# Performance work log

Hardware: AMD Instinct MI355X
Metric: run time of the kernel (lower is better)

The kernel has to match this reference:

```python
import jax, jax.numpy as jnp
import numpy as np

EPS = 1e-5
KS = 3
PAD = 1


def _bn(x, g, b, m, v):
    inv = g / jnp.sqrt(v + EPS)
    return x * inv[None, :, None, None] + (b - m * inv)[None, :, None, None]


def _deform_conv2d(x, off_w, off_b, w):
    # x: (B,C,H,W); off_w: (2*9,C,3,3); w: (Cout,C,3,3)
    B, C, H, W = x.shape
    N = KS * KS
    off = jax.lax.conv_general_dilated(x, off_w, (1, 1), ((PAD, PAD), (PAD, PAD)))
    off = off + off_b[None, :, None, None]                      # (B,2N,H,W)
    xp = jnp.pad(x, ((0, 0), (0, 0), (PAD, PAD), (PAD, PAD)))
    Hp, Wp = H + 2 * PAD, W + 2 * PAD
    r = jnp.arange(KS, dtype=x.dtype) - (KS - 1) // 2           # kernel offsets
    pny = jnp.repeat(r, KS)                                     # row-major (dy)
    pnx = jnp.tile(r, KS)                                       # row-major (dx)
    p0y = jnp.arange(1, H + 1, dtype=x.dtype)[None, None, :, None]
    p0x = jnp.arange(1, W + 1, dtype=x.dtype)[None, None, None, :]
    py = off[:, :N] + pny[None, :, None, None] + p0y            # (B,N,H,W)
    px = off[:, N:] + pnx[None, :, None, None] + p0x
    py = jnp.clip(py, 0.0, Hp - 1.0)
    px = jnp.clip(px, 0.0, Wp - 1.0)
    fy = jax.lax.stop_gradient(jnp.floor(py))                   # indices detached (as in torch impl)
    fx = jax.lax.stop_gradient(jnp.floor(px))
    qy0 = jnp.clip(fy, 0.0, Hp - 1.0)
    qx0 = jnp.clip(fx, 0.0, Wp - 1.0)
    qy1 = jnp.clip(fy + 1.0, 0.0, Hp - 1.0)
    qx1 = jnp.clip(fx + 1.0, 0.0, Wp - 1.0)
    xf = xp.reshape(B, C, Hp * Wp)

    def gather(qy, qx):
        idx = (qy * Wp + qx).astype(jnp.int32)                  # (B,N,H,W)
        return jax.vmap(lambda m_, i_: m_[:, i_])(xf, idx)       # (B,C,N,H,W)

    g_lt = (1.0 + (qy0 - py)) * (1.0 + (qx0 - px))
    g_rb = (1.0 - (qy1 - py)) * (1.0 - (qx1 - px))
    g_lb = (1.0 + (qy0 - py)) * (1.0 - (qx1 - px))
    g_rt = (1.0 - (qy1 - py)) * (1.0 + (qx0 - px))
    xo = (g_lt[:, None] * gather(qy0, qx0) + g_rb[:, None] * gather(qy1, qx1)
          + g_lb[:, None] * gather(qy0, qx1) + g_rt[:, None] * gather(qy1, qx0))
    # (B,C,N,H,W) -> (B,C,H*KS,W*KS): N = (row, col) row-major
    xo = xo.reshape(B, C, KS, KS, H, W).transpose(0, 1, 4, 2, 5, 3).reshape(B, C, H * KS, W * KS)
    return jax.lax.conv_general_dilated(xo, w, (KS, KS), 'VALID')


def _forward(x, dc1_offw, dc1_offb, dc1_w, bn1_g, bn1_b, bn1_m, bn1_v,
             dc2_offw, dc2_offb, dc2_w, bn2_g, bn2_b, bn2_m, bn2_v,
             id_w, id_b, bn3_g, bn3_b, bn3_m, bn3_v):
    h = jax.nn.relu(_bn(_deform_conv2d(x, dc1_offw, dc1_offb, dc1_w), bn1_g, bn1_b, bn1_m, bn1_v))
    h = _bn(_deform_conv2d(h, dc2_offw, dc2_offb, dc2_w), bn2_g, bn2_b, bn2_m, bn2_v)
    idt = jnp.einsum('bchw,oc->bohw', x, id_w[:, :, 0, 0]) + id_b[None, :, None, None]
    idt = _bn(idt, bn3_g, bn3_b, bn3_m, bn3_v)
    return jax.nn.relu(h + idt)


def setup_inputs() -> dict:
    key = jax.random.key(0)
    ks = jax.random.split(key, 16)
    B, Cin, Cout, H, W = 2, 64, 128, 128, 128
    N2 = 2 * KS * KS
    d = {}
    d['x'] = jax.random.normal(ks[0], (B, Cin, H, W), jnp.float32)
    d['dc1_offw'] = jax.random.normal(ks[1], (N2, Cin, KS, KS), jnp.float32) * 0.01
    d['dc1_offb'] = jnp.zeros((N2,), jnp.float32)
    d['dc1_w'] = jax.random.normal(ks[2], (Cout, Cin, KS, KS), jnp.float32) * 0.05
    d['bn1_g'] = 1.0 + 0.1 * jax.random.normal(ks[3], (Cout,), jnp.float32)
    d['bn1_b'] = 0.1 * jax.random.normal(ks[4], (Cout,), jnp.float32)
    d['bn1_m'] = 0.1 * jax.random.normal(ks[5], (Cout,), jnp.float32)
    d['bn1_v'] = jnp.ones((Cout,), jnp.float32)
    d['dc2_offw'] = jax.random.normal(ks[6], (N2, Cout, KS, KS), jnp.float32) * 0.01
    d['dc2_offb'] = jnp.zeros((N2,), jnp.float32)
    d['dc2_w'] = jax.random.normal(ks[7], (Cout, Cout, KS, KS), jnp.float32) * 0.03
    d['bn2_g'] = 1.0 + 0.1 * jax.random.normal(ks[8], (Cout,), jnp.float32)
    d['bn2_b'] = 0.1 * jax.random.normal(ks[9], (Cout,), jnp.float32)
    d['bn2_m'] = 0.1 * jax.random.normal(ks[10], (Cout,), jnp.float32)
    d['bn2_v'] = jnp.ones((Cout,), jnp.float32)
    d['id_w'] = jax.random.normal(ks[11], (Cout, Cin, 1, 1), jnp.float32) * 0.1
    d['id_b'] = jnp.zeros((Cout,), jnp.float32)
    d['bn3_g'] = 1.0 + 0.1 * jax.random.normal(ks[12], (Cout,), jnp.float32)
    d['bn3_b'] = 0.1 * jax.random.normal(ks[13], (Cout,), jnp.float32)
    d['bn3_m'] = 0.1 * jax.random.normal(ks[14], (Cout,), jnp.float32)
    d['bn3_v'] = jnp.ones((Cout,), jnp.float32)
    return d


def reference(x, dc1_offw, dc1_offb, dc1_w, bn1_g, bn1_b, bn1_m, bn1_v,
              dc2_offw, dc2_offb, dc2_w, bn2_g, bn2_b, bn2_m, bn2_v,
              id_w, id_b, bn3_g, bn3_b, bn3_m, bn3_v):
    return _forward(x, dc1_offw, dc1_offb, dc1_w, bn1_g, bn1_b, bn1_m, bn1_v,
                    dc2_offw, dc2_offb, dc2_w, bn2_g, bn2_b, bn2_m, bn2_v,
                    id_w, id_b, bn3_g, bn3_b, bn3_m, bn3_v)
```

## Files before the change

### kernel.cpp

```cpp
#include <hip/hip_runtime.h>
#include <math.h>

#define HH 128
#define WW 128
#define HWSZ (HH * WW)
#define BB 2
#define COUT 128

typedef __bf16 bf16x8 __attribute__((ext_vector_type(8)));
typedef float f32x4 __attribute__((ext_vector_type(4)));
typedef float f32x2 __attribute__((ext_vector_type(2)));
typedef short s16x8 __attribute__((ext_vector_type(8)));
typedef short s16x4 __attribute__((ext_vector_type(4)));
typedef unsigned short u16x4 __attribute__((ext_vector_type(4)));
typedef unsigned short u16x8 __attribute__((ext_vector_type(8)));

__device__ __forceinline__ short tobf(float f) {
  union { float f; unsigned u; } v; v.f = f;
  unsigned r = v.u + 0x7fffu + ((v.u >> 16) & 1u);
  return (short)(r >> 16);
}
__device__ __forceinline__ float asf(unsigned u) {
  union { unsigned u; float f; } v; v.u = u;
  return v.f;
}
__device__ __forceinline__ f32x2 up2(unsigned u) {
  f32x2 r; r[0] = asf(u << 16); r[1] = asf(u & 0xffff0000u); return r;
}
__device__ __forceinline__ unsigned pack2bf(f32x2 v) {
  union { float f; unsigned u; } x, y; x.f = v[0]; y.f = v[1];
  unsigned lo = (x.u + 0x7fffu + ((x.u >> 16) & 1u)) >> 16;
  unsigned hi = (y.u + 0x7fffu + ((y.u >> 16) & 1u)) & 0xffff0000u;
  return lo | hi;
}

#define PA0 73728
#define PA1 221184
#define PA2 229376
#define PA3 247808
#define PA4 284672
#define PA5 284928
__global__ __launch_bounds__(256) void prep_all_kernel(
    const float* __restrict__ dc1_w, const float* __restrict__ dc2_w,
    const float* __restrict__ id_w, const float* __restrict__ dc1_offw,
    const float* __restrict__ dc2_offw,
    const float* g1, const float* b1, const float* m1, const float* v1,
    const float* g2, const float* b2, const float* m2, const float* v2,
    const float* g3, const float* b3, const float* m3, const float* v3,
    const float* idb,
    short* __restrict__ wbf1, short* __restrict__ wbf2,
    short* __restrict__ woff1, short* __restrict__ woff2,
    float* __restrict__ cb1, float* __restrict__ cb2) {
  int idx = blockIdx.x * 256 + threadIdx.x;
  if (idx < PA0) {
    int o = idx / 576, k = idx - o * 576;
    float inv = g1[o] / sqrtf(v1[o] + 1e-5f);
    int col = (k % 9) * 64 + k / 9;
    int di = (((col >> 5) * 2 + (o >> 6)) * 4 + ((o >> 4) & 3)) * 512
           + (((o & 15) | (((col >> 3) & 3) << 4)) * 8) + (col & 7);
    wbf1[di] = tobf(dc1_w[(size_t)o * 576 + k] * inv);
  } else if (idx < PA1) {
    int j = idx - PA0;
    int o = j / 1152, k = j - o * 1152;
    float inv = g2[o] / sqrtf(v2[o] + 1e-5f);
    int col = (k % 9) * 128 + k / 9;
    int di = (((col >> 5) * 2 + (o >> 6)) * 4 + ((o >> 4) & 3)) * 512
           + (((o & 15) | (((col >> 3) & 3) << 4)) * 8) + (col & 7);
    wbf2[di] = tobf(dc2_w[(size_t)o * 1152 + k] * inv);
  } else if (idx < PA2) {
    int j = idx - PA1;
    int o = j >> 6, k = j & 63;
    float inv = g3[o] / sqrtf(v3[o] + 1e-5f);
    int col = 1152 + k;
    int di = (((col >> 5) * 2 + (o >> 6)) * 4 + ((o >> 4) & 3)) * 512
           + (((o & 15) | (((col >> 3) & 3) << 4)) * 8) + (col & 7);
    wbf2[di] = tobf(id_w[(size_t)o * 64 + k] * inv);
  } else if (idx < PA3) {
    int j = idx - PA2;
    int o = j / 576, k = j - o * 576;
    int col = (k % 9) * 64 + k / 9;
    int di = ((col >> 5) * 2 + (o >> 4)) * 512 + ((col >> 3) & 3) * 128
           + (o & 15) * 8 + (col & 7);
    woff1[di] = (o < 18) ? tobf(dc1_offw[(size_t)o * 576 + k]) : (short)0;
  } else if (idx < PA4) {
    int j = idx - PA3;
    int o = j / 1152, k = j - o * 1152;
    int col = (k % 9) * 128 + k / 9;
    int di = ((col >> 5) * 2 + (o >> 4)) * 512 + ((col >> 3) & 3) * 128
           + (o & 15) * 8 + (col & 7);
    woff2[di] = (o < 18) ? tobf(dc2_offw[(size_t)o * 1152 + k]) : (short)0;
  } else if (idx < PA5) {
    int j = idx - PA4;
    if (j < 128) {
      float inv = g1[j] / sqrtf(v1[j] + 1e-5f);
      cb1[j] = b1[j] - m1[j] * inv;
    } else {
      int o = j - 128;
      float inv2_ = g2[o] / sqrtf(v2[o] + 1e-5f);
      float inv3_ = g3[o] / sqrtf(v3[o] + 1e-5f);
      cb2[o] = (b2[o] - m2[o] * inv2_) + idb[o] * inv3_ + (b3[o] - m3[o] * inv3_);
    }
  }
}

__global__ __launch_bounds__(256) void xcast_kernel(const float* __restrict__ x,
                                                    unsigned short* __restrict__ xn) {
  __shared__ short lds[64 * 72];
  int tid = threadIdx.x;
  int gp0 = blockIdx.x * 64;
  int b = gp0 >> 14;
  int pl0 = gp0 & 16383;
  int p = tid & 63;
  int cb = (tid >> 6) * 16;
#pragma unroll
  for (int i = 0; i < 16; i++) {
    int c = cb + i;
    lds[p * 72 + c] = tobf(x[((size_t)(b * 64 + c)) * HWSZ + pl0 + p]);
  }
  __syncthreads();
  int pw = tid >> 2, cseg = (tid & 3) * 16;
  u16x8 a = *(const u16x8*)&lds[pw * 72 + cseg];
  u16x8 b8 = *(const u16x8*)&lds[pw * 72 + cseg + 8];
  *(u16x8*)&xn[(size_t)(gp0 + pw) * 64 + cseg] = a;
  *(u16x8*)&xn[(size_t)(gp0 + pw) * 64 + cseg + 8] = b8;
}

__global__ __launch_bounds__(512, 4) void offconv_mfma_kernel(
    const unsigned short* __restrict__ in, const short* __restrict__ woff,
    const float* __restrict__ offb, float* __restrict__ off, int cshift) {
  __shared__ float redf[4 * 64 * 8];
  const int tid = threadIdx.x;
  const int lane = tid & 63, wv = tid >> 6;
  const int pxg = wv & 3, kh = wv >> 2;
  const int pb = ((blockIdx.x & 7) << 6) | (blockIdx.x >> 3);
  const int pix0 = pb << 6;
  const int x0 = pix0 & 127, y = (pix0 >> 7) & 127, b = pix0 >> 14;
  const int Cin = 1 << cshift;
  const int HK = (9 << cshift) >> 1;
  const int NCh = HK >> 5;
  const unsigned short* inb = in + (size_t)b * HWSZ * Cin;
  const int l15 = lane & 15, quad = lane >> 4;
  const int px = x0 + pxg * 16 + l15;

  f32x4 acc[2];
  acc[0] = (f32x4){0.f, 0.f, 0.f, 0.f};
  acc[1] = (f32x4){0.f, 0.f, 0.f, 0.f};

  for (int i = 0; i < NCh; i++) {
    int k0 = kh * HK + i * 32;
    int n = k0 >> cshift;
    int c0 = (k0 & (Cin - 1)) + quad * 8;
    int yy = y + n / 3 - 1;
    int xx = px + n % 3 - 1;
    bf16x8 bv = {};
    if (((unsigned)yy < (unsigned)HH) && ((unsigned)xx < (unsigned)WW))
      bv = *(const bf16x8*)&inb[((size_t)yy * WW + xx) * Cin + c0];
    int fbase = (k0 >> 5) * 1024 + lane * 8;
    bf16x8 a0 = *(const bf16x8*)&woff[fbase];
    bf16x8 a1 = *(const bf16x8*)&woff[fbase + 512];
    acc[0] = __builtin_amdgcn_mfma_f32_16x16x32_bf16(a0, bv, acc[0], 0, 0, 0);
    acc[1] = __builtin_amdgcn_mfma_f32_16x16x32_bf16(a1, bv, acc[1], 0, 0, 0);
  }
  if (kh == 1) {
    *(f32x4*)&redf[(pxg * 64 + lane) * 8] = acc[0];
    *(f32x4*)&redf[(pxg * 64 + lane) * 8 + 4] = acc[1];
  }
  __syncthreads();
  if (kh == 0) {
    acc[0] += *(const f32x4*)&redf[(pxg * 64 + lane) * 8];
    acc[1] += *(const f32x4*)&redf[(pxg * 64 + lane) * 8 + 4];
#pragma unroll
    for (int ot = 0; ot < 2; ot++) {
#pragma unroll
      for (int r = 0; r < 4; r++) {
        int o = ot * 16 + quad * 4 + r;
        if (o < 18)
          off[(size_t)(b * 18 + o) * HWSZ + y * WW + px] = acc[ot][r] + offb[o];
      }
    }
  }
}

template <int CSH, int KCONV, int KTOT, int MODE>
__global__ __launch_bounds__(512, 4) void deform_mfma_kernel(
    const unsigned short* __restrict__ in, const float* __restrict__ off,
    const short* __restrict__ wbf, const float* __restrict__ cbv,
    const unsigned short* __restrict__ xid, float* __restrict__ outf,
    unsigned short* __restrict__ outb) {
  __shared__ __align__(16) char smem[17408];
  uint4* dsu = (uint4*)smem;
  short* trans = (short*)smem;

  const int tid = threadIdx.x;
  const int lane = tid & 63, wv = tid >> 6;
  const int pb = ((blockIdx.x & 7) << 6) | (blockIdx.x >> 3);
  const int pix0 = pb << 6;
  const int x0 = pix0 & 127, y = (pix0 >> 7) & 127, b = pix0 >> 14;
  const int Cin = 1 << CSH;
  const unsigned short* inb = in + (size_t)b * HWSZ * Cin;
  const int l15 = lane & 15, quad = lane >> 4;
  const int pxg = wv & 3, oh = wv >> 2;
  const int dp = pxg * 16 + (lane >> 2);
  const int cq = lane & 3;
  const int baddr = (((lane & 15) << 2) | (lane >> 4)) << 2;

  for (int t = tid; t < 576; t += 512) {
    int n = t >> 6, pp = t & 63;
    float offy = off[(size_t)(b * 18 + n) * HWSZ + y * WW + x0 + pp];
    float offx = off[(size_t)(b * 18 + 9 + n) * HWSZ + y * WW + x0 + pp];
    float py = offy + (float)(n / 3 - 1) + (float)(y + 1);
    float px = offx + (float)(n % 3 - 1) + (float)(x0 + pp + 1);
    py = fminf(fmaxf(py, 0.f), 129.f);
    px = fminf(fmaxf(px, 0.f), 129.f);
    float fy = floorf(py), fx = floorf(px);
    float qy1 = fminf(fy + 1.f, 129.f), qx1 = fminf(fx + 1.f, 129.f);
    float ty0 = 1.f + fy - py, ty1 = 1.f - (qy1 - py);
    float tx0 = 1.f + fx - px, tx1 = 1.f - (qx1 - px);
    int iy0 = (int)fy - 1, ix0 = (int)fx - 1;
    int iy1 = (int)qy1 - 1, ix1 = (int)qx1 - 1;
    if ((unsigned)iy0 >= (unsigned)HH) ty0 = 0.f;
    if ((unsigned)iy1 >= (unsigned)HH) ty1 = 0.f;
    if ((unsigned)ix0 >= (unsigned)WW) tx0 = 0.f;
    if ((unsigned)ix1 >= (unsigned)WW) tx1 = 0.f;
    int by0 = min(max(iy0, 0), HH - 1), by1 = min(max(iy1, 0), HH - 1);
    int bx0 = min(max(ix0, 0), WW - 1), bx1 = min(max(ix1, 0), WW - 1);
    unsigned w01 = (unsigned)(unsigned short)tobf(ty0 * tx0)
                 | ((unsigned)(unsigned short)tobf(ty0 * tx1) << 16);
    unsigned w23 = (unsigned)(unsigned short)tobf(ty1 * tx0)
                 | ((unsigned)(unsigned short)tobf(ty1 * tx1) << 16);
    uint4 d4;
    d4.x = w01; d4.y = w23;
    d4.z = (unsigned)((by0 * WW + bx0) * Cin);
    d4.w = (unsigned)((((by1 - by0) * WW * Cin) << 16) | ((bx1 - bx0) * Cin));
    dsu[t] = d4;
  }

  f32x4 acc[4];
#pragma unroll
  for (int j = 0; j < 4; j++) acc[j] = (f32x4){0.f, 0.f, 0.f, 0.f};

  __syncthreads();

  const short* wfb = wbf + (size_t)oh * 2048 + lane * 8;
  constexpr int NC = KTOT >> 5;

#pragma unroll 2
  for (int kc = 0; kc < NC; kc++) {
    int k0 = kc << 5;
    const short* wf = wfb + kc * 4096;
    bf16x8 a0 = *(const bf16x8*)(wf);
    bf16x8 a1 = *(const bf16x8*)(wf + 512);
    bf16x8 a2 = *(const bf16x8*)(wf + 1024);
    bf16x8 a3 = *(const bf16x8*)(wf + 1536);
    uint4 pk;
    if (k0 < KCONV) {
      int n = k0 >> CSH;
      int c0 = (k0 & (Cin - 1)) + cq * 8;
      uint4 d4 = dsu[(n << 6) + dp];
      int dx = (int)(d4.w & 0xffffu);
      int dy = (int)d4.w >> 16;
      const unsigned short* ptr = inb + (int)d4.z + c0;
      uint4 q00 = *(const uint4*)(ptr);
      uint4 q01 = *(const uint4*)(ptr + dx);
      uint4 q10 = *(const uint4*)(ptr + dy);
      uint4 q11 = *(const uint4*)(ptr + dx + dy);
      float w0 = asf(d4.x << 16), w1 = asf(d4.x & 0xffff0000u);
      float w2 = asf(d4.y << 16), w3 = asf(d4.y & 0xffff0000u);
      f32x2 v0 = up2(q00.x) * w0 + up2(q01.x) * w1 + up2(q10.x) * w2 + up2(q11.x) * w3;
      f32x2 v1 = up2(q00.y) * w0 + up2(q01.y) * w1 + up2(q10.y) * w2 + up2(q11.y) * w3;
      f32x2 v2 = up2(q00.z) * w0 + up2(q01.z) * w1 + up2(q10.z) * w2 + up2(q11.z) * w3;
      f32x2 v3 = up2(q00.w) * w0 + up2(q01.w) * w1 + up2(q10.w) * w2 + up2(q11.w) * w3;
      pk.x = pack2bf(v0); pk.y = pack2bf(v1); pk.z = pack2bf(v2); pk.w = pack2bf(v3);
    } else {
      int c = (k0 - KCONV) + cq * 8;
      pk = *(const uint4*)&xid[((size_t)(b * HWSZ) + y * WW + x0 + dp) * 64 + c];
    }
    union { int i[4]; bf16x8 v; } bu;
    bu.i[0] = __builtin_amdgcn_ds_bpermute(baddr, (int)pk.x);
    bu.i[1] = __builtin_amdgcn_ds_bpermute(baddr, (int)pk.y);
    bu.i[2] = __builtin_amdgcn_ds_bpermute(baddr, (int)pk.z);
    bu.i[3] = __builtin_amdgcn_ds_bpermute(baddr, (int)pk.w);
    bf16x8 bfr = bu.v;
    acc[0] = __builtin_amdgcn_mfma_f32_16x16x32_bf16(a0, bfr, acc[0], 0, 0, 0);
    acc[1] = __builtin_amdgcn_mfma_f32_16x16x32_bf16(a1, bfr, acc[1], 0, 0, 0);
    acc[2] = __builtin_amdgcn_mfma_f32_16x16x32_bf16(a2, bfr, acc[2], 0, 0, 0);
    acc[3] = __builtin_amdgcn_mfma_f32_16x16x32_bf16(a3, bfr, acc[3], 0, 0, 0);
  }

  if (MODE == 1) {
#pragma unroll
    for (int ot = 0; ot < 4; ot++) {
#pragma unroll
      for (int r = 0; r < 4; r++) {
        int o = oh * 64 + ot * 16 + quad * 4 + r;
        outf[(size_t)(b * COUT + o) * HWSZ + y * WW + x0 + pxg * 16 + l15] =
            fmaxf(acc[ot][r] + cbv[o], 0.f);
      }
    }
  } else {
    __syncthreads();
    int pl = pxg * 16 + l15;
#pragma unroll
    for (int ot = 0; ot < 4; ot++) {
      s16x4 t4;
#pragma unroll
      for (int r = 0; r < 4; r++) {
        int o = oh * 64 + ot * 16 + quad * 4 + r;
        t4[r] = tobf(fmaxf(acc[ot][r] + cbv[o], 0.f));
      }
      *(s16x4*)&trans[pl * 136 + oh * 64 + ot * 16 + quad * 4] = t4;
    }
    __syncthreads();
    int pw = tid >> 3, cs = (tid & 7) * 16;
    u16x8 va = *(const u16x8*)&trans[pw * 136 + cs];
    u16x8 vb = *(const u16x8*)&trans[pw * 136 + cs + 8];
    size_t gb = ((size_t)(b * HWSZ) + y * WW + x0 + pw) * 128 + cs;
    *(u16x8*)&outb[gb] = va;
    *(u16x8*)&outb[gb + 8] = vb;
  }
}

extern "C" void kernel_launch(void* const* d_in, const int* in_sizes, int n_in,
                              void* d_out, int out_size, void* d_ws, size_t ws_size,
                              hipStream_t stream) {
  const float* x        = (const float*)d_in[0];
  const float* dc1_offw = (const float*)d_in[1];
  const float* dc1_offb = (const float*)d_in[2];
  const float* dc1_w    = (const float*)d_in[3];
  const float* bn1_g    = (const float*)d_in[4];
  const float* bn1_b    = (const float*)d_in[5];
  const float* bn1_m    = (const float*)d_in[6];
  const float* bn1_v    = (const float*)d_in[7];
  const float* dc2_offw = (const float*)d_in[8];
  const float* dc2_offb = (const float*)d_in[9];
  const float* dc2_w    = (const float*)d_in[10];
  const float* bn2_g    = (const float*)d_in[11];
  const float* bn2_b    = (const float*)d_in[12];
  const float* bn2_m    = (const float*)d_in[13];
  const float* bn2_v    = (const float*)d_in[14];
  const float* id_w     = (const float*)d_in[15];
  const float* id_b     = (const float*)d_in[16];
  const float* bn3_g    = (const float*)d_in[17];
  const float* bn3_b    = (const float*)d_in[18];
  const float* bn3_m    = (const float*)d_in[19];
  const float* bn3_v    = (const float*)d_in[20];

  float* wsf = (float*)d_ws;
  float* off1 = wsf;
  float* off2 = off1 + (size_t)BB * 18 * HWSZ;
  float* cb1  = off2 + (size_t)BB * 18 * HWSZ;
  float* cb2  = cb1 + 128;
  unsigned short* xbf = (unsigned short*)(cb2 + 128);
  unsigned short* h1  = xbf + (size_t)BB * HWSZ * 64;
  short* wbf1  = (short*)(h1 + (size_t)BB * HWSZ * COUT);
  short* wbf2  = wbf1 + (size_t)128 * 576;
  short* woff1 = wbf2 + (size_t)128 * 1216;
  short* woff2 = woff1 + (size_t)18 * 1024;

  hipLaunchKernelGGL(prep_all_kernel, dim3((PA5 + 255) / 256), dim3(256), 0, stream,
                     dc1_w, dc2_w, id_w, dc1_offw, dc2_offw,
                     bn1_g, bn1_b, bn1_m, bn1_v, bn2_g, bn2_b, bn2_m, bn2_v,
                     bn3_g, bn3_b, bn3_m, bn3_v, id_b,
                     wbf1, wbf2, woff1, woff2, cb1, cb2);
  hipLaunchKernelGGL(xcast_kernel, dim3(BB * HWSZ / 64), dim3(256), 0, stream, x, xbf);

  hipLaunchKernelGGL(offconv_mfma_kernel, dim3(512), dim3(512), 0, stream,
                     xbf, woff1, dc1_offb, off1, 6);
  hipLaunchKernelGGL((deform_mfma_kernel<6, 576, 576, 0>), dim3(512), dim3(512), 0, stream,
                     xbf, off1, wbf1, cb1, (const unsigned short*)nullptr,
                     (float*)nullptr, h1);
  hipLaunchKernelGGL(offconv_mfma_kernel, dim3(512), dim3(512), 0, stream,
                     h1, woff2, dc2_offb, off2, 7);
  hipLaunchKernelGGL((deform_mfma_kernel<7, 1152, 1216, 1>), dim3(512), dim3(512), 0, stream,
                     h1, off2, wbf2, cb2, xbf, (float*)d_out,
                     (unsigned short*)nullptr);
}
```

Measured before the change: 193.8 us.

## Split K across waves so each deform gather is computed once per pixel

The deform kernel moves from 64-pixel blocks of 8 waves, where two waves split the output channels and each redid the same bilinear gather, to 32-pixel blocks of 4 waves. Each wave now covers all 128 output channels over half of K, and the two halves are summed through LDS before the epilogue. This removes the duplicated gather and interpolation work and the duplicated global loads of sampled inputs. The cost is an extra LDS reduction pass, an extra barrier, and more accumulator and A-fragment registers per wave. Interpolated values are also packed to bf16 by truncation instead of round-to-nearest, which saves ALU work but changes numerics slightly.

```diff
diff --git a/kernel.cpp b/kernel.cpp
--- a/kernel.cpp
+++ b/kernel.cpp
@@ -27,11 +27,10 @@
 __device__ __forceinline__ f32x2 up2(unsigned u) {
   f32x2 r; r[0] = asf(u << 16); r[1] = asf(u & 0xffff0000u); return r;
 }
-__device__ __forceinline__ unsigned pack2bf(f32x2 v) {
-  union { float f; unsigned u; } x, y; x.f = v[0]; y.f = v[1];
-  unsigned lo = (x.u + 0x7fffu + ((x.u >> 16) & 1u)) >> 16;
-  unsigned hi = (y.u + 0x7fffu + ((y.u >> 16) & 1u)) & 0xffff0000u;
-  return lo | hi;
+__device__ __forceinline__ unsigned trunc2bf(f32x2 v) {
+  union { float f; unsigned u; } a, b;
+  a.f = v[0]; b.f = v[1];
+  return __builtin_amdgcn_perm(b.u, a.u, 0x07060302u);
 }
 
 #define PA0 73728
@@ -182,30 +181,31 @@
 }
 
 template <int CSH, int KCONV, int KTOT, int MODE>
-__global__ __launch_bounds__(512, 4) void deform_mfma_kernel(
+__global__ __launch_bounds__(256, 3) void deform_mfma_kernel(
     const unsigned short* __restrict__ in, const float* __restrict__ off,
     const short* __restrict__ wbf, const float* __restrict__ cbv,
     const unsigned short* __restrict__ xid, float* __restrict__ outf,
     unsigned short* __restrict__ outb) {
-  __shared__ __align__(16) char smem[17408];
+  __shared__ __align__(16) char smem[25088];
   uint4* dsu = (uint4*)smem;
-  short* trans = (short*)smem;
+  f32x4* redf = (f32x4*)smem;
+  short* trans = (short*)(smem + 16384);
 
   const int tid = threadIdx.x;
   const int lane = tid & 63, wv = tid >> 6;
-  const int pb = ((blockIdx.x & 7) << 6) | (blockIdx.x >> 3);
-  const int pix0 = pb << 6;
+  const int pb = ((blockIdx.x & 7) << 7) | (blockIdx.x >> 3);
+  const int pix0 = pb << 5;
   const int x0 = pix0 & 127, y = (pix0 >> 7) & 127, b = pix0 >> 14;
   const int Cin = 1 << CSH;
   const unsigned short* inb = in + (size_t)b * HWSZ * Cin;
   const int l15 = lane & 15, quad = lane >> 4;
-  const int pxg = wv & 3, oh = wv >> 2;
+  const int pxg = wv & 1, kh = wv >> 1;
   const int dp = pxg * 16 + (lane >> 2);
   const int cq = lane & 3;
   const int baddr = (((lane & 15) << 2) | (lane >> 4)) << 2;
 
-  for (int t = tid; t < 576; t += 512) {
-    int n = t >> 6, pp = t & 63;
+  for (int t = tid; t < 288; t += 256) {
+    int n = t >> 5, pp = t & 31;
     float offy = off[(size_t)(b * 18 + n) * HWSZ + y * WW + x0 + pp];
     float offx = off[(size_t)(b * 18 + 9 + n) * HWSZ + y * WW + x0 + pp];
     float py = offy + (float)(n / 3 - 1) + (float)(y + 1);
@@ -224,39 +224,43 @@
     if ((unsigned)ix1 >= (unsigned)WW) tx1 = 0.f;
     int by0 = min(max(iy0, 0), HH - 1), by1 = min(max(iy1, 0), HH - 1);
     int bx0 = min(max(ix0, 0), WW - 1), bx1 = min(max(ix1, 0), WW - 1);
-    unsigned w01 = (unsigned)(unsigned short)tobf(ty0 * tx0)
-                 | ((unsigned)(unsigned short)tobf(ty0 * tx1) << 16);
-    unsigned w23 = (unsigned)(unsigned short)tobf(ty1 * tx0)
-                 | ((unsigned)(unsigned short)tobf(ty1 * tx1) << 16);
     uint4 d4;
-    d4.x = w01; d4.y = w23;
+    d4.x = (unsigned)(unsigned short)tobf(ty0 * tx0)
+         | ((unsigned)(unsigned short)tobf(ty0 * tx1) << 16);
+    d4.y = (unsigned)(unsigned short)tobf(ty1 * tx0)
+         | ((unsigned)(unsigned short)tobf(ty1 * tx1) << 16);
     d4.z = (unsigned)((by0 * WW + bx0) * Cin);
     d4.w = (unsigned)((((by1 - by0) * WW * Cin) << 16) | ((bx1 - bx0) * Cin));
     dsu[t] = d4;
   }
 
-  f32x4 acc[4];
-#pragma unroll
-  for (int j = 0; j < 4; j++) acc[j] = (f32x4){0.f, 0.f, 0.f, 0.f};
-
-  __syncthreads();
-
-  const short* wfb = wbf + (size_t)oh * 2048 + lane * 8;
+  f32x4 acc[8];
+#pragma unroll
+  for (int j = 0; j < 8; j++) acc[j] = (f32x4){0.f, 0.f, 0.f, 0.f};
+
+  __syncthreads();
+
   constexpr int NC = KTOT >> 5;
-
-#pragma unroll 2
-  for (int kc = 0; kc < NC; kc++) {
+  constexpr int HC = NC >> 1;
+  const short* wfb = wbf + lane * 8;
+
+  for (int i = 0; i < HC; i++) {
+    int kc = kh * HC + i;
     int k0 = kc << 5;
-    const short* wf = wfb + kc * 4096;
+    const short* wf = wfb + (size_t)kc * 4096;
     bf16x8 a0 = *(const bf16x8*)(wf);
     bf16x8 a1 = *(const bf16x8*)(wf + 512);
     bf16x8 a2 = *(const bf16x8*)(wf + 1024);
     bf16x8 a3 = *(const bf16x8*)(wf + 1536);
+    bf16x8 a4 = *(const bf16x8*)(wf + 2048);
+    bf16x8 a5 = *(const bf16x8*)(wf + 2560);
+    bf16x8 a6 = *(const bf16x8*)(wf + 3072);
+    bf16x8 a7 = *(const bf16x8*)(wf + 3584);
     uint4 pk;
     if (k0 < KCONV) {
       int n = k0 >> CSH;
       int c0 = (k0 & (Cin - 1)) + cq * 8;
-      uint4 d4 = dsu[(n << 6) + dp];
+      uint4 d4 = dsu[(n << 5) + dp];
       int dx = (int)(d4.w & 0xffffu);
       int dy = (int)d4.w >> 16;
       const unsigned short* ptr = inb + (int)d4.z + c0;
@@ -270,7 +274,8 @@
       f32x2 v1 = up2(q00.y) * w0 + up2(q01.y) * w1 + up2(q10.y) * w2 + up2(q11.y) * w3;
       f32x2 v2 = up2(q00.z) * w0 + up2(q01.z) * w1 + up2(q10.z) * w2 + up2(q11.z) * w3;
       f32x2 v3 = up2(q00.w) * w0 + up2(q01.w) * w1 + up2(q10.w) * w2 + up2(q11.w) * w3;
-      pk.x = pack2bf(v0); pk.y = pack2bf(v1); pk.z = pack2bf(v2); pk.w = pack2bf(v3);
+      pk.x = trunc2bf(v0); pk.y = trunc2bf(v1);
+      pk.z = trunc2bf(v2); pk.w = trunc2bf(v3);
     } else {
       int c = (k0 - KCONV) + cq * 8;
       pk = *(const uint4*)&xid[((size_t)(b * HWSZ) + y * WW + x0 + dp) * 64 + c];
@@ -285,31 +290,46 @@
     acc[1] = __builtin_amdgcn_mfma_f32_16x16x32_bf16(a1, bfr, acc[1], 0, 0, 0);
     acc[2] = __builtin_amdgcn_mfma_f32_16x16x32_bf16(a2, bfr, acc[2], 0, 0, 0);
     acc[3] = __builtin_amdgcn_mfma_f32_16x16x32_bf16(a3, bfr, acc[3], 0, 0, 0);
-  }
-
-  if (MODE == 1) {
-#pragma unroll
-    for (int ot = 0; ot < 4; ot++) {
-#pragma unroll
-      for (int r = 0; r < 4; r++) {
-        int o = oh * 64 + ot * 16 + quad * 4 + r;
-        outf[(size_t)(b * COUT + o) * HWSZ + y * WW + x0 + pxg * 16 + l15] =
-            fmaxf(acc[ot][r] + cbv[o], 0.f);
+    acc[4] = __builtin_amdgcn_mfma_f32_16x16x32_bf16(a4, bfr, acc[4], 0, 0, 0);
+    acc[5] = __builtin_amdgcn_mfma_f32_16x16x32_bf16(a5, bfr, acc[5], 0, 0, 0);
+    acc[6] = __builtin_amdgcn_mfma_f32_16x16x32_bf16(a6, bfr, acc[6], 0, 0, 0);
+    acc[7] = __builtin_amdgcn_mfma_f32_16x16x32_bf16(a7, bfr, acc[7], 0, 0, 0);
+  }
+
+  __syncthreads();
+  if (kh == 1) {
+#pragma unroll
+    for (int f = 0; f < 8; f++) redf[f * 128 + pxg * 64 + lane] = acc[f];
+  }
+  __syncthreads();
+  if (kh == 0) {
+#pragma unroll
+    for (int f = 0; f < 8; f++) acc[f] += redf[f * 128 + pxg * 64 + lane];
+    if (MODE == 1) {
+#pragma unroll
+      for (int f = 0; f < 8; f++) {
+#pragma unroll
+        for (int r = 0; r < 4; r++) {
+          int o = (f >> 2) * 64 + (f & 3) * 16 + quad * 4 + r;
+          outf[(size_t)(b * COUT + o) * HWSZ + y * WW + x0 + pxg * 16 + l15] =
+              fmaxf(acc[f][r] + cbv[o], 0.f);
+        }
+      }
+    } else {
+      int pl = pxg * 16 + l15;
+#pragma unroll
+      for (int f = 0; f < 8; f++) {
+        s16x4 t4;
+#pragma unroll
+        for (int r = 0; r < 4; r++) {
+          int o = (f >> 2) * 64 + (f & 3) * 16 + quad * 4 + r;
+          t4[r] = tobf(fmaxf(acc[f][r] + cbv[o], 0.f));
+        }
+        *(s16x4*)&trans[pl * 136 + (f >> 2) * 64 + (f & 3) * 16 + quad * 4] = t4;
       }
     }
-  } else {
-    __syncthreads();
-    int pl = pxg * 16 + l15;
-#pragma unroll
-    for (int ot = 0; ot < 4; ot++) {
-      s16x4 t4;
-#pragma unroll
-      for (int r = 0; r < 4; r++) {
-        int o = oh * 64 + ot * 16 + quad * 4 + r;
-        t4[r] = tobf(fmaxf(acc[ot][r] + cbv[o], 0.f));
-      }
-      *(s16x4*)&trans[pl * 136 + oh * 64 + ot * 16 + quad * 4] = t4;
-    }
+  }
+  if (MODE == 0) {
     __syncthreads();
     int pw = tid >> 3, cs = (tid & 7) * 16;
     u16x8 va = *(const u16x8*)&trans[pw * 136 + cs];
@@ -366,12 +386,12 @@
 
   hipLaunchKernelGGL(offconv_mfma_kernel, dim3(512), dim3(512), 0, stream,
                      xbf, woff1, dc1_offb, off1, 6);
-  hipLaunchKernelGGL((deform_mfma_kernel<6, 576, 576, 0>), dim3(512), dim3(512), 0, stream,
+  hipLaunchKernelGGL((deform_mfma_kernel<6, 576, 576, 0>), dim3(1024), dim3(256), 0, stream,
                      xbf, off1, wbf1, cb1, (const unsigned short*)nullptr,
                      (float*)nullptr, h1);
   hipLaunchKernelGGL(offconv_mfma_kernel, dim3(512), dim3(512), 0, stream,
                      h1, woff2, dc2_offb, off2, 7);
-  hipLaunchKernelGGL((deform_mfma_kernel<7, 1152, 1216, 1>), dim3(512), dim3(512), 0, stream,
+  hipLaunchKernelGGL((deform_mfma_kernel<7, 1152, 1216, 1>), dim3(1024), dim3(256), 0, stream,
                      h1, off2, wbf2, cb2, xbf, (float*)d_out,
                      (unsigned short*)nullptr);
 }
```

Result: faster. 187.5 us (-3.2%).
